# Kernel tuning notes

Measured on AMD Instinct MI355X. Metric: run time of the kernel, lower is better.

## Reference

```python
import jax, jax.numpy as jnp
import numpy as np
import math

NUM_ROTATIONS = 8
STRIDE = 1
PADDING = 1


def _rotate_weights(weight, num_rotations):
    """Bilinear rotation of conv filters, matching torch affine_grid/grid_sample
    with align_corners=False and zero padding.

    weight: (O, I, k, k) -> returns (R, O, I, k, k)
    """
    O, I, k, _ = weight.shape
    dt = weight.dtype
    # align_corners=False normalized pixel-center coords in [-1, 1]
    c = (2.0 * jnp.arange(k, dtype=jnp.float32) + 1.0) / k - 1.0
    ygrid, xgrid = jnp.meshgrid(c, c, indexing='ij')          # (k, k)
    angles = 2.0 * math.pi * jnp.arange(num_rotations, dtype=jnp.float32) / num_rotations
    cos = jnp.cos(angles)[:, None, None]                       # (R,1,1)
    sin = jnp.sin(angles)[:, None, None]
    # theta = [[cos, -sin, 0], [sin, cos, 0]] applied to (x, y, 1)
    xs = cos * xgrid - sin * ygrid                             # (R,k,k)
    ys = sin * xgrid + cos * ygrid
    # unnormalize (align_corners=False): ix = ((x+1)*W - 1)/2
    ix = ((xs + 1.0) * k - 1.0) * 0.5
    iy = ((ys + 1.0) * k - 1.0) * 0.5
    ix0f = jnp.floor(ix); iy0f = jnp.floor(iy)
    wx1 = (ix - ix0f).astype(dt); wy1 = (iy - iy0f).astype(dt)
    wx0 = 1.0 - wx1; wy0 = 1.0 - wy1
    ix0 = ix0f.astype(jnp.int32); iy0 = iy0f.astype(jnp.int32)
    ix1 = ix0 + 1; iy1 = iy0 + 1

    def gather(iyc, ixc):
        valid = ((iyc >= 0) & (iyc < k) & (ixc >= 0) & (ixc < k)).astype(dt)
        iycl = jnp.clip(iyc, 0, k - 1)
        ixcl = jnp.clip(ixc, 0, k - 1)
        # advanced indexing broadcasts: (O, I, R, k, k)
        return weight[:, :, iycl, ixcl] * valid

    out = (gather(iy0, ix0) * (wy0 * wx0)
           + gather(iy0, ix1) * (wy0 * wx1)
           + gather(iy1, ix0) * (wy1 * wx0)
           + gather(iy1, ix1) * (wy1 * wx1))                   # (O,I,R,k,k)
    return jnp.transpose(out, (2, 0, 1, 3, 4))                 # (R,O,I,k,k)


def setup_inputs() -> dict:
    key = jax.random.key(0)
    k1, k2 = jax.random.split(key)
    x = jax.random.normal(k1, (4, 256, 128, 128), dtype=jnp.float32)
    weight = jax.random.normal(k2, (256, 256, 3, 3), dtype=jnp.float32)
    return {"x": x, "weight": weight}


def reference(x, weight):
    R = NUM_ROTATIONS
    O, I, k, _ = weight.shape
    rw = _rotate_weights(weight, R)                            # (R,O,I,k,k)
    rw_flat = rw.reshape(R * O, I, k, k)
    # one conv for all rotations (same input), then max over rotations
    out = jax.lax.conv_general_dilated(
        x, rw_flat,
        window_strides=(STRIDE, STRIDE),
        padding=[(PADDING, PADDING), (PADDING, PADDING)],
        dimension_numbers=('NCHW', 'OIHW', 'NCHW'))           # (B, R*O, H', W')
    B, _, Hp, Wp = out.shape
    out = out.reshape(B, R, O, Hp, Wp)
    return jnp.max(out, axis=1)                                # (B, O, H', W')
```

## Files before the change

### kernel.cpp

```cpp
#include <hip/hip_runtime.h>
#include <hip/hip_bf16.h>
#include <math.h>

typedef __attribute__((ext_vector_type(8))) short bf16x8;
typedef __attribute__((ext_vector_type(4))) float f32x4;

#define R_TOTAL 8
#define CIN     256
#define COUT    256
#define HH      128
#define WW      128
#define BB      4
#define MTOT    (COUT * R_TOTAL)
#define KTAPS   9

#define XROWS 4
#define XSZ   (XROWS * 130 * 32)
#define ABUF  (128 * 32)

__device__ __forceinline__ void g2l16(void* lds, const void* g) {
    __builtin_amdgcn_global_load_lds(
        (const __attribute__((address_space(1))) unsigned int*)g,
        (__attribute__((address_space(3))) unsigned int*)lds,
        16, 0, 0);
}

__global__ __launch_bounds__(256)
void to_nhwc_bf16(const float* __restrict__ x, __hip_bfloat16* __restrict__ xb) {
    __shared__ __hip_bfloat16 t[32][33];
    const int b  = blockIdx.z;
    const int c0 = blockIdx.y * 32;
    const int p0 = blockIdx.x * 32;
    const int tx = threadIdx.x & 31;
    const int ty = threadIdx.x >> 5;
    const float* xp = x + (size_t)b * CIN * (HH * WW);
    #pragma unroll
    for (int j = 0; j < 4; ++j) {
        int c = ty * 4 + j;
        t[c][tx] = __float2bfloat16(xp[(size_t)(c0 + c) * (HH * WW) + p0 + tx]);
    }
    __syncthreads();
    __hip_bfloat16* op = xb + ((size_t)b * (HH * WW) + p0) * CIN + c0;
    #pragma unroll
    for (int j = 0; j < 4; ++j) {
        int p = ty * 4 + j;
        op[(size_t)p * CIN + tx] = t[tx][p];
    }
}

__global__ __launch_bounds__(256)
void zero_guard_row(__hip_bfloat16* __restrict__ xb) {
    size_t base = (size_t)BB * HH * WW * CIN;
    int i = blockIdx.x * 256 + threadIdx.x;
    xb[base + i] = __float2bfloat16(0.0f);
}

__global__ __launch_bounds__(256)
void rotate_weights_bf16(const float* __restrict__ w, __hip_bfloat16* __restrict__ rwb) {
    const int i = threadIdx.x;
    const int m = blockIdx.x;
    const int o = m >> 3, r = m & 7;

    float ang = 6.283185307179586f * (float)r / 8.0f;
    float cs = cosf(ang), sn = sinf(ang);

    const float* wp = w + ((size_t)o * CIN + i) * 9;
    __hip_bfloat16* op = rwb + (size_t)m * (KTAPS * CIN) + i;

    #pragma unroll
    for (int ky = 0; ky < 3; ++ky) {
        #pragma unroll
        for (int kx = 0; kx < 3; ++kx) {
            float yg = (2.0f * (float)ky + 1.0f) / 3.0f - 1.0f;
            float xg = (2.0f * (float)kx + 1.0f) / 3.0f - 1.0f;
            float xsf = cs * xg - sn * yg;
            float ysf = sn * xg + cs * yg;
            float ix = ((xsf + 1.0f) * 3.0f - 1.0f) * 0.5f;
            float iy = ((ysf + 1.0f) * 3.0f - 1.0f) * 0.5f;
            float ix0f = floorf(ix), iy0f = floorf(iy);
            float wx1 = ix - ix0f,  wy1 = iy - iy0f;
            float wx0 = 1.0f - wx1, wy0 = 1.0f - wy1;
            int ix0 = (int)ix0f, iy0 = (int)iy0f;
            int ix1 = ix0 + 1,   iy1 = iy0 + 1;
            float acc = 0.0f;
            if (iy0 >= 0 && iy0 < 3 && ix0 >= 0 && ix0 < 3) acc += wp[iy0*3+ix0] * (wy0*wx0);
            if (iy0 >= 0 && iy0 < 3 && ix1 >= 0 && ix1 < 3) acc += wp[iy0*3+ix1] * (wy0*wx1);
            if (iy1 >= 0 && iy1 < 3 && ix0 >= 0 && ix0 < 3) acc += wp[iy1*3+ix0] * (wy1*wx0);
            if (iy1 >= 0 && iy1 < 3 && ix1 >= 0 && ix1 < 3) acc += wp[iy1*3+ix1] * (wy1*wx1);
            op[(ky * 3 + kx) * CIN] = __float2bfloat16(acc);
        }
    }
}

__global__ __launch_bounds__(512)
void rotconv_mfma_kernel(const __hip_bfloat16* __restrict__ xb,
                         const __hip_bfloat16* __restrict__ rwb,
                         float* __restrict__ out) {
    const int tid  = threadIdx.x;
    const int lane = tid & 63;
    const int w    = tid >> 6;
    const int wm   = w >> 2;
    const int wn   = w & 3;
    const int q    = lane >> 4, lr = lane & 15;

    const int bid = (blockIdx.x & 7) * 512 + (blockIdx.x >> 3);
    const int mt  = bid >> 8;
    const int nt  = bid & 255;
    const int b   = nt >> 6;
    const int y0  = (nt & 63) * 2;
    const int m0  = mt << 7;

    __shared__ __align__(16) __hip_bfloat16 xs[2 * XSZ];
    __shared__ __align__(16) __hip_bfloat16 As[4 * ABUF];

    {
        int bufi = tid >> 8;
        int rem  = tid & 255;
        int row = rem >> 6; int colsel = (rem >> 5) & 1; int ch = rem & 31;
        int colL = colsel ? 129 : 0;
        xs[bufi * XSZ + (row * 130 + colL) * 32 + ch] = __float2bfloat16(0.0f);
    }

    int aOff[4];
    #pragma unroll
    for (int mi = 0; mi < 4; ++mi) {
        int row = wm * 64 + mi * 16 + lr;
        aOff[mi] = row * 32 + 8 * (q ^ ((row >> 1) & 3));
    }
    int bOff[4][3];
    #pragma unroll
    for (int ni = 0; ni < 4; ++ni) {
        int pbase = wn * 64 + ni * 16;
        int ir = pbase >> 7;
        int col = (pbase & 127) + lr;
        #pragma unroll
        for (int kx = 0; kx < 3; ++kx) {
            int colL = col + kx;
            bOff[ni][kx] = (ir * 130 + colL) * 32 + 8 * (q ^ ((colL >> 1) & 3));
        }
    }

    const int arow = w * 16 + (lane >> 2);
    const int dstA = (w * 16) * 32;
    const __hip_bfloat16* srcA =
        rwb + (size_t)(m0 + arow) * (KTAPS * CIN) + 8 * ((lane & 3) ^ ((arow >> 1) & 3));

    const __hip_bfloat16* srcX[4];
    int dstX[4];
    #pragma unroll
    for (int j = 0; j < 4; ++j) {
        int id = j * 8 + w;
        int row = id >> 3;
        int cg  = (id & 7) * 16;
        int gy = y0 - 1 + row;
        size_t rowIdx = ((unsigned)gy < (unsigned)HH) ? (size_t)(b * HH + gy)
                                                      : (size_t)(BB * HH);
        int gx = cg + (lane >> 2);
        int colL = gx + 1;
        dstX[j] = (row * 130 + 1 + cg) * 32;
        srcX[j] = xb + (rowIdx * WW + gx) * CIN + 8 * ((lane & 3) ^ ((colL >> 1) & 3));
    }

    f32x4 acc[4][4];
    #pragma unroll
    for (int mi = 0; mi < 4; ++mi)
        #pragma unroll
        for (int ni = 0; ni < 4; ++ni) {
            f32x4 z = {0.f, 0.f, 0.f, 0.f};
            acc[mi][ni] = z;
        }

    __syncthreads();

    #pragma unroll
    for (int j = 0; j < 4; ++j) g2l16(xs + dstX[j], srcX[j]);
    __builtin_amdgcn_sched_barrier(0);
    g2l16(As + 0 * ABUF + dstA, srcA + 0 * CIN);
    __builtin_amdgcn_sched_barrier(0);
    g2l16(As + 1 * ABUF + dstA, srcA + 1 * CIN);

#define TAP(C, P, NW, DOA, DOX)                                                \
  {                                                                            \
    if (DOA) {                                                                 \
      g2l16(As + ((9*(C)+(P)+2) & 3) * ABUF + dstA,                            \
            srcA + ((9*(C)+(P)+2) % 9) * CIN + ((9*(C)+(P)+2) / 9) * 32);      \
    }                                                                          \
    if (DOX) {                                                                 \
      g2l16(xs + (((C)+1) & 1) * XSZ + dstX[(P)-2],                            \
            srcX[(P)-2] + ((C)+1) * 32);                                       \
    }                                                                          \
    asm volatile("s_waitcnt vmcnt(%0)" :: "i"(NW) : "memory");                 \
    asm volatile("s_barrier" ::: "memory");                                    \
    {                                                                          \
      const __hip_bfloat16* ar = As + ((9*(C)+(P)) & 3) * ABUF;                \
      const __hip_bfloat16* br = xs + ((C) & 1) * XSZ + ((P)/3) * (130 * 32);  \
      bf16x8 af[4], bv[4];                                                     \
      _Pragma("unroll")                                                        \
      for (int mi = 0; mi < 4; ++mi) af[mi] = *(const bf16x8*)(ar + aOff[mi]); \
      _Pragma("unroll")                                                        \
      for (int ni = 0; ni < 4; ++ni)                                           \
          bv[ni] = *(const bf16x8*)(br + bOff[ni][(P) % 3]);                   \
      __builtin_amdgcn_s_setprio(1);                                           \
      _Pragma("unroll")                                                        \
      for (int mi = 0; mi < 4; ++mi)                                           \
          _Pragma("unroll")                                                    \
          for (int ni = 0; ni < 4; ++ni)                                       \
              acc[mi][ni] = __builtin_amdgcn_mfma_f32_16x16x32_bf16(           \
                  af[mi], bv[ni], acc[mi][ni], 0, 0, 0);                       \
      __builtin_amdgcn_s_setprio(0);                                           \
    }                                                                          \
  }

#define CHUNK_MID(C)                                                           \
    TAP(C, 0, 2, 1, 0) TAP(C, 1, 2, 1, 0) TAP(C, 2, 3, 1, 1)                   \
    TAP(C, 3, 4, 1, 1) TAP(C, 4, 4, 1, 1) TAP(C, 5, 4, 1, 1)                   \
    TAP(C, 6, 3, 1, 0) TAP(C, 7, 2, 1, 0) TAP(C, 8, 2, 1, 0)

    CHUNK_MID(0) CHUNK_MID(1) CHUNK_MID(2) CHUNK_MID(3)
    CHUNK_MID(4) CHUNK_MID(5) CHUNK_MID(6)
    TAP(7, 0, 2, 1, 0) TAP(7, 1, 2, 1, 0) TAP(7, 2, 2, 1, 0)
    TAP(7, 3, 2, 1, 0) TAP(7, 4, 2, 1, 0) TAP(7, 5, 2, 1, 0)
    TAP(7, 6, 2, 1, 0) TAP(7, 7, 1, 0, 0) TAP(7, 8, 0, 0, 0)

#undef TAP
#undef CHUNK_MID

    const int oBase = (m0 + wm * 64) >> 3;
    #pragma unroll
    for (int mi = 0; mi < 4; ++mi) {
        #pragma unroll
        for (int ni = 0; ni < 4; ++ni) {
            f32x4 a4 = acc[mi][ni];
            float v = fmaxf(fmaxf(a4[0], a4[1]), fmaxf(a4[2], a4[3]));
            v = fmaxf(v, __shfl_xor(v, 16));
            if ((q & 1) == 0) {
                int o = oBase + mi * 2 + (q >> 1);
                int p = wn * 64 + ni * 16 + lr;
                int y = y0 + (p >> 7);
                int colc = p & 127;
                out[(((size_t)(b * COUT + o)) * HH + y) * WW + colc] = v;
            }
        }
    }
}

__global__ void rotate_weights_kernel(const float* __restrict__ w,
                                      float* __restrict__ rw,
                                      int r0, int rcount) {
    int idx = blockIdx.x * blockDim.x + threadIdx.x;
    int total = COUT * CIN * rcount;
    if (idx >= total) return;
    int rr = idx % rcount;
    int ii = (idx / rcount) % CIN;
    int oo = idx / (rcount * CIN);
    int r  = r0 + rr;
    float ang = 6.283185307179586f * (float)r / 8.0f;
    float cs = cosf(ang), sn = sinf(ang);
    const float* wp = w  + ((size_t)oo * CIN + ii) * 9;
    float*       op = rw + (((size_t)oo * CIN + ii) * rcount + rr) * 9;
    #pragma unroll
    for (int ky = 0; ky < 3; ++ky)
        #pragma unroll
        for (int kx = 0; kx < 3; ++kx) {
            float yg = (2.0f * ky + 1.0f) / 3.0f - 1.0f;
            float xg = (2.0f * kx + 1.0f) / 3.0f - 1.0f;
            float xsf = cs * xg - sn * yg;
            float ysf = sn * xg + cs * yg;
            float ix = ((xsf + 1.0f) * 3.0f - 1.0f) * 0.5f;
            float iy = ((ysf + 1.0f) * 3.0f - 1.0f) * 0.5f;
            float ix0f = floorf(ix), iy0f = floorf(iy);
            float wx1 = ix - ix0f,  wy1 = iy - iy0f;
            float wx0 = 1.0f - wx1, wy0 = 1.0f - wy1;
            int ix0 = (int)ix0f, iy0 = (int)iy0f;
            int ix1 = ix0 + 1,   iy1 = iy0 + 1;
            float acc = 0.0f;
            if (iy0 >= 0 && iy0 < 3 && ix0 >= 0 && ix0 < 3) acc += wp[iy0*3+ix0]*(wy0*wx0);
            if (iy0 >= 0 && iy0 < 3 && ix1 >= 0 && ix1 < 3) acc += wp[iy0*3+ix1]*(wy0*wx1);
            if (iy1 >= 0 && iy1 < 3 && ix0 >= 0 && ix0 < 3) acc += wp[iy1*3+ix0]*(wy1*wx0);
            if (iy1 >= 0 && iy1 < 3 && ix1 >= 0 && ix1 < 3) acc += wp[iy1*3+ix1]*(wy1*wx1);
            op[ky * 3 + kx] = acc;
        }
}

template <int RCOUNT>
__global__ __launch_bounds__(256)
void rotconv_max_kernel(const float* __restrict__ x,
                        const float* __restrict__ rw,
                        float* __restrict__ out,
                        int first) {
    const int tid = threadIdx.x;
    const int tx = tid & 15;
    const int ty = tid >> 4;
    const int x0 = blockIdx.x * 32;
    const int y0 = blockIdx.y * 32;
    const int o  = blockIdx.z % COUT;
    const int b  = blockIdx.z / COUT;
    __shared__ float xsm[34][36];
    float acc[RCOUNT][2][2];
    #pragma unroll
    for (int r = 0; r < RCOUNT; ++r)
        #pragma unroll
        for (int py = 0; py < 2; ++py)
            #pragma unroll
            for (int px = 0; px < 2; ++px) acc[r][py][px] = 0.0f;
    for (int i = 0; i < CIN; ++i) {
        __syncthreads();
        const float* xp = x + ((size_t)(b * CIN + i)) * (HH * WW);
        for (int idx = tid; idx < 34 * 34; idx += 256) {
            int row = idx / 34, col = idx - row * 34;
            int gy = y0 - 1 + row, gx = x0 - 1 + col;
            float v = 0.0f;
            if (gy >= 0 && gy < HH && gx >= 0 && gx < WW) v = xp[gy * WW + gx];
            xsm[row][col] = v;
        }
        __syncthreads();
        float xv[4][4];
        #pragma unroll
        for (int ry = 0; ry < 4; ++ry)
            #pragma unroll
            for (int cx = 0; cx < 4; ++cx) xv[ry][cx] = xsm[ty*2+ry][tx*2+cx];
        const float* wp = rw + ((size_t)(o * CIN + i)) * (RCOUNT * 9);
        #pragma unroll
        for (int r = 0; r < RCOUNT; ++r) {
            float wv[9];
            #pragma unroll
            for (int t2 = 0; t2 < 9; ++t2) wv[t2] = wp[r * 9 + t2];
            #pragma unroll
            for (int py = 0; py < 2; ++py)
                #pragma unroll
                for (int px = 0; px < 2; ++px) {
                    float a = acc[r][py][px];
                    #pragma unroll
                    for (int ky = 0; ky < 3; ++ky)
                        #pragma unroll
                        for (int kx = 0; kx < 3; ++kx)
                            a += xv[py+ky][px+kx] * wv[ky*3+kx];
                    acc[r][py][px] = a;
                }
        }
    }
    #pragma unroll
    for (int py = 0; py < 2; ++py)
        #pragma unroll
        for (int px = 0; px < 2; ++px) {
            float m = acc[0][py][px];
            #pragma unroll
            for (int r = 1; r < RCOUNT; ++r) m = fmaxf(m, acc[r][py][px]);
            int oy = y0 + ty * 2 + py;
            int ox = x0 + tx * 2 + px;
            float* op = out + (((size_t)(b * COUT + o)) * HH + oy) * WW + ox;
            if (first) *op = m;
            else       *op = fmaxf(*op, m);
        }
}

extern "C" void kernel_launch(void* const* d_in, const int* in_sizes, int n_in,
                              void* d_out, int out_size, void* d_ws, size_t ws_size,
                              hipStream_t stream) {
    const float* x = (const float*)d_in[0];
    const float* w = (const float*)d_in[1];
    float* out = (float*)d_out;

    const size_t xbBytes = ((size_t)BB * HH * WW + WW) * CIN * sizeof(__hip_bfloat16);
    const size_t rwBytes = (size_t)MTOT * KTAPS * CIN * sizeof(__hip_bfloat16);

    if (ws_size >= xbBytes + rwBytes) {
        __hip_bfloat16* xbuf = (__hip_bfloat16*)d_ws;
        __hip_bfloat16* rwb  = (__hip_bfloat16*)((char*)d_ws + xbBytes);

        to_nhwc_bf16<<<dim3((HH * WW) / 32, CIN / 32, BB), 256, 0, stream>>>(x, xbuf);
        zero_guard_row<<<(WW * CIN) / 256, 256, 0, stream>>>(xbuf);
        rotate_weights_bf16<<<MTOT, 256, 0, stream>>>(w, rwb);
        rotconv_mfma_kernel<<<4096, 512, 0, stream>>>(xbuf, rwb, out);
        return;
    }

    float* rw = (float*)d_ws;
    int chunk = 8;
    while (chunk > 1 && (size_t)COUT * CIN * chunk * 9 * sizeof(float) > ws_size)
        chunk >>= 1;
    int first = 1;
    for (int r0 = 0; r0 < R_TOTAL; r0 += chunk) {
        int rc = chunk;
        int total = COUT * CIN * rc;
        rotate_weights_kernel<<<(total + 255) / 256, 256, 0, stream>>>(w, rw, r0, rc);
        dim3 grid(WW / 32, HH / 32, BB * COUT);
        switch (rc) {
            case 8: rotconv_max_kernel<8><<<grid, 256, 0, stream>>>(x, rw, out, first); break;
            case 4: rotconv_max_kernel<4><<<grid, 256, 0, stream>>>(x, rw, out, first); break;
            case 2: rotconv_max_kernel<2><<<grid, 256, 0, stream>>>(x, rw, out, first); break;
            default: rotconv_max_kernel<1><<<grid, 256, 0, stream>>>(x, rw, out, first); break;
        }
        first = 0;
    }
}
```

Before: 587.0 us.

## Enlarge conv tile to four output rows per block with 128x512 MFMA tile

Each block now computes four output image rows instead of two, doubling the N tile to 512 pixels while keeping 128 rotated-filter rows. The input halo buffer grows from 4 to 6 rows, so each weight tile is reused across twice as many pixels and the halo overhead per output row shrinks. Each wave now holds 4x8 accumulator tiles, doubling register pressure; the launch bound requests 2 blocks per SM, and the grid halves to 2048 blocks. The fully unrolled channel-chunk sequence is turned into a partially rolled loop over chunk groups, which may cut code size but adds a runtime channel offset.

```diff
diff --git a/kernel.cpp b/kernel.cpp
--- a/kernel.cpp
+++ b/kernel.cpp
@@ -14,8 +14,8 @@
 #define MTOT    (COUT * R_TOTAL)
 #define KTAPS   9
 
-#define XROWS 4
-#define XSZ   (XROWS * 130 * 32)
+#define XRW   6
+#define XSZ   (XRW * 130 * 32)
 #define ABUF  (128 * 32)
 
 __device__ __forceinline__ void g2l16(void* lds, const void* g) {
@@ -92,7 +92,7 @@
     }
 }
 
-__global__ __launch_bounds__(512)
+__global__ __launch_bounds__(512, 2)
 void rotconv_mfma_kernel(const __hip_bfloat16* __restrict__ xb,
                          const __hip_bfloat16* __restrict__ rwb,
                          float* __restrict__ out) {
@@ -103,20 +103,20 @@
     const int wn   = w & 3;
     const int q    = lane >> 4, lr = lane & 15;
 
-    const int bid = (blockIdx.x & 7) * 512 + (blockIdx.x >> 3);
-    const int mt  = bid >> 8;
-    const int nt  = bid & 255;
-    const int b   = nt >> 6;
-    const int y0  = (nt & 63) * 2;
+    const int bid = (blockIdx.x & 7) * 256 + (blockIdx.x >> 3);
+    const int mt  = bid >> 7;
+    const int nt  = bid & 127;
+    const int b   = nt >> 5;
+    const int y0  = (nt & 31) * 4;
     const int m0  = mt << 7;
 
     __shared__ __align__(16) __hip_bfloat16 xs[2 * XSZ];
     __shared__ __align__(16) __hip_bfloat16 As[4 * ABUF];
 
-    {
-        int bufi = tid >> 8;
-        int rem  = tid & 255;
-        int row = rem >> 6; int colsel = (rem >> 5) & 1; int ch = rem & 31;
+    for (int j = tid; j < 2 * XRW * 2 * 32; j += 512) {
+        int bufi = j / (XRW * 2 * 32);
+        int rem  = j % (XRW * 2 * 32);
+        int row = rem / 64; int colsel = (rem >> 5) & 1; int ch = rem & 31;
         int colL = colsel ? 129 : 0;
         xs[bufi * XSZ + (row * 130 + colL) * 32 + ch] = __float2bfloat16(0.0f);
     }
@@ -127,45 +127,38 @@
         int row = wm * 64 + mi * 16 + lr;
         aOff[mi] = row * 32 + 8 * (q ^ ((row >> 1) & 3));
     }
-    int bOff[4][3];
-    #pragma unroll
-    for (int ni = 0; ni < 4; ++ni) {
-        int pbase = wn * 64 + ni * 16;
-        int ir = pbase >> 7;
-        int col = (pbase & 127) + lr;
+    int bOff[8][3];
+    #pragma unroll
+    for (int ni = 0; ni < 8; ++ni)
         #pragma unroll
         for (int kx = 0; kx < 3; ++kx) {
-            int colL = col + kx;
-            bOff[ni][kx] = (ir * 130 + colL) * 32 + 8 * (q ^ ((colL >> 1) & 3));
-        }
-    }
+            int colL = ni * 16 + lr + kx;
+            bOff[ni][kx] = (wn * 130 + colL) * 32 + 8 * (q ^ ((colL >> 1) & 3));
+        }
 
     const int arow = w * 16 + (lane >> 2);
     const int dstA = (w * 16) * 32;
     const __hip_bfloat16* srcA =
         rwb + (size_t)(m0 + arow) * (KTAPS * CIN) + 8 * ((lane & 3) ^ ((arow >> 1) & 3));
 
-    const __hip_bfloat16* srcX[4];
-    int dstX[4];
-    #pragma unroll
-    for (int j = 0; j < 4; ++j) {
-        int id = j * 8 + w;
-        int row = id >> 3;
-        int cg  = (id & 7) * 16;
-        int gy = y0 - 1 + row;
+    const __hip_bfloat16* srcX[6];
+    int dstX[6];
+    #pragma unroll
+    for (int j = 0; j < 6; ++j) {
+        int gy = y0 - 1 + j;
         size_t rowIdx = ((unsigned)gy < (unsigned)HH) ? (size_t)(b * HH + gy)
                                                       : (size_t)(BB * HH);
-        int gx = cg + (lane >> 2);
+        int gx = w * 16 + (lane >> 2);
         int colL = gx + 1;
-        dstX[j] = (row * 130 + 1 + cg) * 32;
+        dstX[j] = (j * 130 + 1 + w * 16) * 32;
         srcX[j] = xb + (rowIdx * WW + gx) * CIN + 8 * ((lane & 3) ^ ((colL >> 1) & 3));
     }
 
-    f32x4 acc[4][4];
+    f32x4 acc[4][8];
     #pragma unroll
     for (int mi = 0; mi < 4; ++mi)
         #pragma unroll
-        for (int ni = 0; ni < 4; ++ni) {
+        for (int ni = 0; ni < 8; ++ni) {
             f32x4 z = {0.f, 0.f, 0.f, 0.f};
             acc[mi][ni] = z;
         }
@@ -173,72 +166,93 @@
     __syncthreads();
 
     #pragma unroll
-    for (int j = 0; j < 4; ++j) g2l16(xs + dstX[j], srcX[j]);
+    for (int j = 0; j < 6; ++j) g2l16(xs + dstX[j], srcX[j]);
     __builtin_amdgcn_sched_barrier(0);
     g2l16(As + 0 * ABUF + dstA, srcA + 0 * CIN);
     __builtin_amdgcn_sched_barrier(0);
     g2l16(As + 1 * ABUF + dstA, srcA + 1 * CIN);
 
-#define TAP(C, P, NW, DOA, DOX)                                                \
-  {                                                                            \
-    if (DOA) {                                                                 \
-      g2l16(As + ((9*(C)+(P)+2) & 3) * ABUF + dstA,                            \
-            srcA + ((9*(C)+(P)+2) % 9) * CIN + ((9*(C)+(P)+2) / 9) * 32);      \
-    }                                                                          \
-    if (DOX) {                                                                 \
-      g2l16(xs + (((C)+1) & 1) * XSZ + dstX[(P)-2],                            \
-            srcX[(P)-2] + ((C)+1) * 32);                                       \
-    }                                                                          \
-    asm volatile("s_waitcnt vmcnt(%0)" :: "i"(NW) : "memory");                 \
-    asm volatile("s_barrier" ::: "memory");                                    \
+#define TAPCORE(J, P)                                                          \
     {                                                                          \
-      const __hip_bfloat16* ar = As + ((9*(C)+(P)) & 3) * ABUF;                \
-      const __hip_bfloat16* br = xs + ((C) & 1) * XSZ + ((P)/3) * (130 * 32);  \
-      bf16x8 af[4], bv[4];                                                     \
+      const __hip_bfloat16* ar = As + (((J) + (P)) & 3) * ABUF;                \
+      const __hip_bfloat16* br = xs + ((J) & 1) * XSZ + ((P) / 3) * (130*32);  \
+      bf16x8 af[4];                                                            \
       _Pragma("unroll")                                                        \
       for (int mi = 0; mi < 4; ++mi) af[mi] = *(const bf16x8*)(ar + aOff[mi]); \
       _Pragma("unroll")                                                        \
-      for (int ni = 0; ni < 4; ++ni)                                           \
-          bv[ni] = *(const bf16x8*)(br + bOff[ni][(P) % 3]);                   \
-      __builtin_amdgcn_s_setprio(1);                                           \
-      _Pragma("unroll")                                                        \
-      for (int mi = 0; mi < 4; ++mi)                                           \
+      for (int h = 0; h < 2; ++h) {                                            \
+        bf16x8 bv[4];                                                          \
+        _Pragma("unroll")                                                      \
+        for (int nj = 0; nj < 4; ++nj)                                         \
+            bv[nj] = *(const bf16x8*)(br + bOff[h * 4 + nj][(P) % 3]);         \
+        __builtin_amdgcn_s_setprio(1);                                         \
+        _Pragma("unroll")                                                      \
+        for (int mi = 0; mi < 4; ++mi)                                         \
           _Pragma("unroll")                                                    \
-          for (int ni = 0; ni < 4; ++ni)                                       \
-              acc[mi][ni] = __builtin_amdgcn_mfma_f32_16x16x32_bf16(           \
-                  af[mi], bv[ni], acc[mi][ni], 0, 0, 0);                       \
-      __builtin_amdgcn_s_setprio(0);                                           \
-    }                                                                          \
+          for (int nj = 0; nj < 4; ++nj)                                       \
+            acc[mi][h * 4 + nj] = __builtin_amdgcn_mfma_f32_16x16x32_bf16(     \
+                af[mi], bv[nj], acc[mi][h * 4 + nj], 0, 0, 0);                 \
+        __builtin_amdgcn_s_setprio(0);                                         \
+      }                                                                        \
+    }
+
+#define TAPS(J, P, NW, DOX)                                                    \
+  {                                                                            \
+    g2l16(As + (((J) + (P) + 2) & 3) * ABUF + dstA,                            \
+          srcA + (((P) + 2) % 9) * CIN + (c + ((P) + 2) / 9) * 32);            \
+    if (DOX) g2l16(xs + (((J) + 1) & 1) * XSZ + dstX[(P) ? (P) - 1 : 0],       \
+                   srcX[(P) ? (P) - 1 : 0] + (c + 1) * 32);                    \
+    asm volatile("s_waitcnt vmcnt(%0)" :: "i"(NW) : "memory");                 \
+    asm volatile("s_barrier" ::: "memory");                                    \
+    TAPCORE(J, P)                                                              \
   }
 
-#define CHUNK_MID(C)                                                           \
-    TAP(C, 0, 2, 1, 0) TAP(C, 1, 2, 1, 0) TAP(C, 2, 3, 1, 1)                   \
-    TAP(C, 3, 4, 1, 1) TAP(C, 4, 4, 1, 1) TAP(C, 5, 4, 1, 1)                   \
-    TAP(C, 6, 3, 1, 0) TAP(C, 7, 2, 1, 0) TAP(C, 8, 2, 1, 0)
-
-    CHUNK_MID(0) CHUNK_MID(1) CHUNK_MID(2) CHUNK_MID(3)
-    CHUNK_MID(4) CHUNK_MID(5) CHUNK_MID(6)
-    TAP(7, 0, 2, 1, 0) TAP(7, 1, 2, 1, 0) TAP(7, 2, 2, 1, 0)
-    TAP(7, 3, 2, 1, 0) TAP(7, 4, 2, 1, 0) TAP(7, 5, 2, 1, 0)
-    TAP(7, 6, 2, 1, 0) TAP(7, 7, 1, 0, 0) TAP(7, 8, 0, 0, 0)
-
-#undef TAP
-#undef CHUNK_MID
+#define TAPT(J, P, NW)                                                         \
+  {                                                                            \
+    if ((P) <= 6)                                                              \
+      g2l16(As + (((J) + (P) + 2) & 3) * ABUF + dstA,                          \
+            srcA + (((P) + 2) % 9) * CIN + (c + ((P) + 2) / 9) * 32);          \
+    asm volatile("s_waitcnt vmcnt(%0)" :: "i"(NW) : "memory");                 \
+    asm volatile("s_barrier" ::: "memory");                                    \
+    TAPCORE(J, P)                                                              \
+  }
+
+#define CHKS(J)                                                                \
+    TAPS(J, 0, 2, 0) TAPS(J, 1, 3, 1) TAPS(J, 2, 4, 1) TAPS(J, 3, 4, 1)        \
+    TAPS(J, 4, 4, 1) TAPS(J, 5, 4, 1) TAPS(J, 6, 4, 1) TAPS(J, 7, 3, 0)        \
+    TAPS(J, 8, 2, 0)
+
+#define CHKT(J)                                                                \
+    TAPT(J, 0, 2) TAPT(J, 1, 2) TAPT(J, 2, 2) TAPT(J, 3, 2) TAPT(J, 4, 2)      \
+    TAPT(J, 5, 2) TAPT(J, 6, 2) TAPT(J, 7, 1) TAPT(J, 8, 0)
+
+    for (int cb = 0; cb < 8; cb += 4) {
+        { const int c = cb + 0; CHKS(0) }
+        { const int c = cb + 1; CHKS(1) }
+        { const int c = cb + 2; CHKS(2) }
+        if (cb == 0) { const int c = 3; CHKS(3) }
+        else         { const int c = 7; CHKT(3) }
+    }
+
+#undef TAPCORE
+#undef TAPS
+#undef TAPT
+#undef CHKS
+#undef CHKT
 
     const int oBase = (m0 + wm * 64) >> 3;
+    const int yOut  = y0 + wn;
     #pragma unroll
     for (int mi = 0; mi < 4; ++mi) {
         #pragma unroll
-        for (int ni = 0; ni < 4; ++ni) {
+        for (int ni = 0; ni < 8; ++ni) {
             f32x4 a4 = acc[mi][ni];
             float v = fmaxf(fmaxf(a4[0], a4[1]), fmaxf(a4[2], a4[3]));
             v = fmaxf(v, __shfl_xor(v, 16));
             if ((q & 1) == 0) {
                 int o = oBase + mi * 2 + (q >> 1);
-                int p = wn * 64 + ni * 16 + lr;
-                int y = y0 + (p >> 7);
-                int colc = p & 127;
-                out[(((size_t)(b * COUT + o)) * HH + y) * WW + colc] = v;
+                int colc = ni * 16 + lr;
+                out[(((size_t)(b * COUT + o)) * HH + yOut) * WW + colc] = v;
             }
         }
     }
@@ -371,7 +385,7 @@
         to_nhwc_bf16<<<dim3((HH * WW) / 32, CIN / 32, BB), 256, 0, stream>>>(x, xbuf);
         zero_guard_row<<<(WW * CIN) / 256, 256, 0, stream>>>(xbuf);
         rotate_weights_bf16<<<MTOT, 256, 0, stream>>>(w, rwb);
-        rotconv_mfma_kernel<<<4096, 512, 0, stream>>>(xbuf, rwb, out);
+        rotconv_mfma_kernel<<<2048, 512, 0, stream>>>(xbuf, rwb, out);
         return;
     }
 
```

Result: slower. 880.2 us (+49.9%).
